# Kernel tuning notes

Measured on AMD Instinct MI355X. Metric: run time of the kernel, lower is better.

Reference implementation:

```python
import jax, jax.numpy as jnp
import numpy as np

MODEL_DIM = 2048
NUM_HEADS = 32
HEAD_DIM = 64
NUM_KV_HEADS = 8
ROPE_BASE = 10000.0
BATCH = 2
SEQ = 2048


def setup_inputs() -> dict:
    key = jax.random.key(0)
    ks = jax.random.split(key, 5)
    sd = 1.0 / np.sqrt(MODEL_DIM)
    x = jax.random.normal(ks[0], (BATCH, SEQ, MODEL_DIM), dtype=jnp.float32)
    Wq = jax.random.normal(ks[1], (MODEL_DIM, NUM_HEADS * HEAD_DIM), dtype=jnp.float32) * sd
    Wk = jax.random.normal(ks[2], (MODEL_DIM, NUM_KV_HEADS * HEAD_DIM), dtype=jnp.float32) * sd
    Wv = jax.random.normal(ks[3], (MODEL_DIM, NUM_KV_HEADS * HEAD_DIM), dtype=jnp.float32) * sd
    Wo = jax.random.normal(ks[4], (NUM_HEADS * HEAD_DIM, MODEL_DIM), dtype=jnp.float32) * sd
    return {"x": x, "Wq": Wq, "Wk": Wk, "Wv": Wv, "Wo": Wo}


def _rope_cache(seq_len, head_dim, base, dtype):
    # inv_freq over even dims, standard rotate-half (Llama-style) RoPE cache
    inv_freq = 1.0 / (base ** (jnp.arange(0, head_dim, 2, dtype=jnp.float32) / head_dim))
    t = jnp.arange(seq_len, dtype=jnp.float32)
    freqs = jnp.outer(t, inv_freq)               # [S, hd/2]
    emb = jnp.concatenate([freqs, freqs], axis=-1)  # [S, hd]
    return jnp.cos(emb).astype(dtype), jnp.sin(emb).astype(dtype)


def _rotate_half(x):
    h = x.shape[-1] // 2
    return jnp.concatenate([-x[..., h:], x[..., :h]], axis=-1)


def _apply_rope(q, k, cos, sin):
    # q,k: [B, H, S, hd]; cos,sin: [S, hd] -> broadcast over batch/heads
    cos = cos[None, None, :, :]
    sin = sin[None, None, :, :]
    q = q * cos + _rotate_half(q) * sin
    k = k * cos + _rotate_half(k) * sin
    return q, k


def reference(x, Wq, Wk, Wv, Wo):
    bsz, seq_len, _ = x.shape
    q_per_kv = NUM_HEADS // NUM_KV_HEADS

    # projections -> [B, H, S, hd]
    q = (x @ Wq).reshape(bsz, seq_len, NUM_HEADS, HEAD_DIM).transpose(0, 2, 1, 3)
    k = (x @ Wk).reshape(bsz, seq_len, NUM_KV_HEADS, HEAD_DIM).transpose(0, 2, 1, 3)
    v = (x @ Wv).reshape(bsz, seq_len, NUM_KV_HEADS, HEAD_DIM).transpose(0, 2, 1, 3)

    # GQA: repeat_interleave KV heads to match Q heads
    k = jnp.repeat(k, q_per_kv, axis=1)
    v = jnp.repeat(v, q_per_kv, axis=1)

    cos, sin = _rope_cache(seq_len, HEAD_DIM, ROPE_BASE, x.dtype)
    q, k = _apply_rope(q, k, cos, sin)

    scale = 1.0 / np.sqrt(HEAD_DIM)
    scores = jnp.einsum('bhqd,bhkd->bhqk', q, k) * scale  # [B,H,S,S]
    causal = jnp.tril(jnp.ones((seq_len, seq_len), dtype=bool))
    scores = jnp.where(causal[None, None], scores, jnp.finfo(scores.dtype).min)
    attn = jax.nn.softmax(scores, axis=-1)
    y = jnp.einsum('bhqk,bhkd->bhqd', attn, v)  # [B,H,S,hd]

    y = y.transpose(0, 2, 1, 3).reshape(bsz, seq_len, NUM_HEADS * HEAD_DIM)
    return y @ Wo
```

## Files before the change

kernel.cpp:

```cpp
#include <hip/hip_runtime.h>
#include <cstdint>

typedef unsigned short u16;
typedef __attribute__((ext_vector_type(8))) short short8;
typedef __attribute__((ext_vector_type(4))) short short4v;
typedef __attribute__((ext_vector_type(4))) float f32x4;

#define SEQ     2048
#define NHEADS  32
#define NKV     8
#define HD      64
#define DM      2048
#define MROWS   4096
#define KVSTR   1024
#define PSTR    88

__device__ __forceinline__ float b2f(unsigned int u) {
    return __builtin_bit_cast(float, u << 16);
}
__device__ __forceinline__ u16 f2b(float f) {
    unsigned int u = __builtin_bit_cast(unsigned int, f);
    return (u16)((u + 0x7fffu + ((u >> 16) & 1u)) >> 16);
}

__device__ __forceinline__ float dpp_red_max16(float x) {
    int v = __builtin_bit_cast(int, x);
    x = fmaxf(x, __builtin_bit_cast(float,
        __builtin_amdgcn_update_dpp(v, v, 0xB1, 0xF, 0xF, true)));
    v = __builtin_bit_cast(int, x);
    x = fmaxf(x, __builtin_bit_cast(float,
        __builtin_amdgcn_update_dpp(v, v, 0x4E, 0xF, 0xF, true)));
    v = __builtin_bit_cast(int, x);
    x = fmaxf(x, __builtin_bit_cast(float,
        __builtin_amdgcn_update_dpp(v, v, 0x141, 0xF, 0xF, true)));
    v = __builtin_bit_cast(int, x);
    x = fmaxf(x, __builtin_bit_cast(float,
        __builtin_amdgcn_update_dpp(v, v, 0x140, 0xF, 0xF, true)));
    return x;
}
__device__ __forceinline__ float dpp_red_sum16(float x) {
    int v = __builtin_bit_cast(int, x);
    x = x + __builtin_bit_cast(float,
        __builtin_amdgcn_update_dpp(v, v, 0xB1, 0xF, 0xF, true));
    v = __builtin_bit_cast(int, x);
    x = x + __builtin_bit_cast(float,
        __builtin_amdgcn_update_dpp(v, v, 0x4E, 0xF, 0xF, true));
    v = __builtin_bit_cast(int, x);
    x = x + __builtin_bit_cast(float,
        __builtin_amdgcn_update_dpp(v, v, 0x141, 0xF, 0xF, true));
    v = __builtin_bit_cast(int, x);
    x = x + __builtin_bit_cast(float,
        __builtin_amdgcn_update_dpp(v, v, 0x140, 0xF, 0xF, true));
    return x;
}

#define GLOAD_LDS16(g, l)                                              \
    __builtin_amdgcn_global_load_lds(                                  \
        (const __attribute__((address_space(1))) void*)(g),            \
        (__attribute__((address_space(3))) void*)(l), 16, 0, 0)

__global__ __launch_bounds__(256) void cvt_f32_bf16(
    const float* __restrict__ in, u16* __restrict__ out, int n4) {
    int i = blockIdx.x * 256 + threadIdx.x;
    if (i < n4) {
        float4 v = ((const float4*)in)[i];
        ushort4 o;
        o.x = f2b(v.x); o.y = f2b(v.y); o.z = f2b(v.z); o.w = f2b(v.w);
        ((ushort4*)out)[i] = o;
    }
}

__global__ __launch_bounds__(256) void rope_table_kernel(
    float* __restrict__ cosT, float* __restrict__ sinT) {
    int idx = blockIdx.x * 256 + threadIdx.x;
    int s  = idx >> 5;
    int dl = idx & 31;
    float inv_freq = exp2f((float)dl * -0.41524101186092025f);
    float ang = (float)s * inv_freq;
    float sn, cs;
    sincosf(ang, &sn, &cs);
    cosT[idx] = cs;
    sinT[idx] = sn;
}

__global__ __launch_bounds__(256) void transpose_f32_bf16(
    const float* __restrict__ in, u16* __restrict__ out, int K, int N) {
    __shared__ float tile[32][33];
    int n0 = blockIdx.x * 32, k0 = blockIdx.y * 32;
    int tx = threadIdx.x, ty = threadIdx.y;
    for (int r = ty; r < 32; r += 8)
        tile[r][tx] = in[(size_t)(k0 + r) * N + n0 + tx];
    __syncthreads();
    for (int r = ty; r < 32; r += 8)
        out[(size_t)(n0 + r) * K + k0 + tx] = f2b(tile[tx][r]);
}

#define GEMM_BODY(A, BT, Kdim)                                             \
    constexpr int BK = 32;                                                 \
    __shared__ __align__(16) u16 As[128 * BK];                             \
    __shared__ __align__(16) u16 Bs[128 * BK];                             \
    const int tid  = threadIdx.x;                                          \
    const int wid  = tid >> 6;                                             \
    const int lane = tid & 63;                                             \
    const int quad = lane >> 4;                                            \
    const int l16  = lane & 15;                                            \
    const int rowBase = blockIdx.y * 128;                                  \
    const int colBase = blockIdx.x * 128;                                  \
    const int wr = (wid >> 1) * 64;                                        \
    const int wc = (wid & 1) * 64;                                         \
    const int srow = wid * 32 + (lane >> 2);                               \
    const int scol = (lane & 3) * 8;                                       \
    const u16* gA = (A)  + (size_t)(rowBase + srow) * (Kdim) + scol;       \
    const u16* gB = (BT) + (size_t)(colBase + srow) * (Kdim) + scol;       \
    u16* lA0 = &As[(wid * 32) * BK];                                       \
    u16* lA1 = &As[(wid * 32 + 16) * BK];                                  \
    u16* lB0 = &Bs[(wid * 32) * BK];                                       \
    u16* lB1 = &Bs[(wid * 32 + 16) * BK];                                  \
    const size_t row16 = (size_t)16 * (Kdim);                              \
    f32x4 acc[4][4] = {};                                                  \
    for (int k0 = 0; k0 < (Kdim); k0 += BK) {                              \
        GLOAD_LDS16(gA + k0,         lA0);                                 \
        GLOAD_LDS16(gA + k0 + row16, lA1);                                 \
        GLOAD_LDS16(gB + k0,         lB0);                                 \
        GLOAD_LDS16(gB + k0 + row16, lB1);                                 \
        __syncthreads();                                                   \
        short8 a[4], b[4];                                                 \
        _Pragma("unroll")                                                  \
        for (int mi = 0; mi < 4; ++mi)                                     \
            a[mi] = *(const short8*)&As[(wr + mi * 16 + l16) * BK + quad * 8]; \
        _Pragma("unroll")                                                  \
        for (int ni = 0; ni < 4; ++ni)                                     \
            b[ni] = *(const short8*)&Bs[(wc + ni * 16 + l16) * BK + quad * 8]; \
        _Pragma("unroll")                                                  \
        for (int mi = 0; mi < 4; ++mi)                                     \
            _Pragma("unroll")                                              \
            for (int ni = 0; ni < 4; ++ni)                                 \
                acc[mi][ni] = __builtin_amdgcn_mfma_f32_16x16x32_bf16(     \
                    a[mi], b[ni], acc[mi][ni], 0, 0, 0);                   \
        __syncthreads();                                                   \
    }                                                                      \
    const int wRow = rowBase + wr;                                         \
    const int wCol = colBase + wc;

__global__ __launch_bounds__(256) void gemm_qkv(
    const u16* __restrict__ A, const u16* __restrict__ BT,
    u16* __restrict__ Qb, u16* __restrict__ KVb,
    const float* __restrict__ cosT, const float* __restrict__ sinT) {
    GEMM_BODY(A, BT, DM)

    u16* dst;
    int dstride, dcol;
    float scale;
    bool doRope;
    if (wCol < 2048)      { dst = Qb;  dstride = 2048; dcol = wCol;        scale = 0.125f; doRope = true;  }
    else if (wCol < 2560) { dst = KVb; dstride = 1024; dcol = wCol - 2048; scale = 1.0f;   doRope = true;  }
    else                  { dst = KVb; dstride = 1024; dcol = wCol - 2048; scale = 1.0f;   doRope = false; }

#pragma unroll
    for (int mi = 0; mi < 4; ++mi) {
#pragma unroll
        for (int r = 0; r < 4; ++r) {
            const int R = wRow + mi * 16 + quad * 4 + r;
            u16* crow = dst + (size_t)R * dstride + dcol;
            if (doRope) {
                const int s = R & (SEQ - 1);
#pragma unroll
                for (int ni = 0; ni < 2; ++ni) {
                    const int dl = ni * 16 + l16;
                    float lo = acc[mi][ni][r];
                    float hi = acc[mi][ni + 2][r];
                    float cs = cosT[s * 32 + dl];
                    float sn = sinT[s * 32 + dl];
                    crow[dl]      = f2b((lo * cs - hi * sn) * scale);
                    crow[dl + 32] = f2b((hi * cs + lo * sn) * scale);
                }
            } else {
#pragma unroll
                for (int ni = 0; ni < 4; ++ni)
                    crow[ni * 16 + l16] = f2b(acc[mi][ni][r]);
            }
        }
    }
}

__global__ __launch_bounds__(256) void gemm_out(
    const u16* __restrict__ A, const u16* __restrict__ BT,
    float* __restrict__ C32) {
    GEMM_BODY(A, BT, DM)
#pragma unroll
    for (int mi = 0; mi < 4; ++mi) {
#pragma unroll
        for (int r = 0; r < 4; ++r) {
            const int R = wRow + mi * 16 + quad * 4 + r;
            float* crow = C32 + (size_t)R * DM + wCol;
#pragma unroll
            for (int ni = 0; ni < 4; ++ni)
                crow[ni * 16 + l16] = acc[mi][ni][r];
        }
    }
}

__global__ __launch_bounds__(512, 4) void flash_attn(
    const u16* __restrict__ Q, const u16* __restrict__ KV,
    u16* __restrict__ Yb, float* __restrict__ PoA,
    float* __restrict__ Ml) {
    __shared__ __align__(16) u16 Ks[64 * 64];
    __shared__ __align__(16) u16 Vt[64 * 72];
    __shared__ __align__(16) u16 Ps[8 * 16 * PSTR];

    const int p   = blockIdx.x >> 1;
    const int sh  = blockIdx.x & 1;
    const int h   = blockIdx.y;
    const int b   = blockIdx.z;
    const int kvh = h >> 2;
    const int tid  = threadIdx.x;
    const int wid  = tid >> 6;
    const int lane = tid & 63;
    const int quad = lane >> 4;
    const int l16  = lane & 15;

    const u16* Kg = KV + (size_t)b * SEQ * KVSTR + kvh * HD;
    const u16* Vg = Kg + 512;
    u16* Psw = Ps + wid * 16 * PSTR;

    const int kKey = tid >> 3, kCc = tid & 7;
    const int vkp  = tid & 31;
    const int vd0  = (tid >> 5) * 4;

    for (int ph = 0; ph < 2; ++ph) {
        const int qt = ph ? (15 - p) : p;
        const int hc = ph ? (16 - p) : (p + 1);
        const int tS = sh * hc;
        const int rowBaseW = qt * 128 + wid * 16;

        short8 qf[2];
#pragma unroll
        for (int ks = 0; ks < 2; ++ks)
            qf[ks] = *(const short8*)&Q[
                (size_t)(b * SEQ + rowBaseW + l16) * (NHEADS * HD)
                + h * HD + ks * 32 + quad * 8];

        f32x4 o[4] = {};
        float mi[4], li[4];
#pragma unroll
        for (int r = 0; r < 4; ++r) { mi[r] = -3e38f; li[r] = 0.f; }

        const size_t jF = (size_t)tS * 64;
        short8  kreg = *(const short8*)&Kg[(jF + kKey) * KVSTR + kCc * 8];
        short4v vrA  = *(const short4v*)&Vg[(jF + 2 * vkp)     * KVSTR + vd0];
        short4v vrB  = *(const short4v*)&Vg[(jF + 2 * vkp + 1) * KVSTR + vd0];

        for (int tt = 0; tt < hc; ++tt) {
            const int j0 = (tS + tt) * 64;
            __syncthreads();

            *(short8*)&Ks[kKey * 64 + ((kCc ^ (kKey & 7)) * 8)] = kreg;
#pragma unroll
            for (int i = 0; i < 4; ++i) {
                unsigned int w = (unsigned int)(u16)vrA[i]
                               | ((unsigned int)(u16)vrB[i] << 16);
                ((unsigned int*)Vt)[(vd0 + i) * 36 + vkp] = w;
            }
            __syncthreads();

            if (tt + 1 < hc) {
                const size_t jn = (size_t)(j0 + 64);
                kreg = *(const short8*)&Kg[(jn + kKey) * KVSTR + kCc * 8];
                vrA  = *(const short4v*)&Vg[(jn + 2 * vkp)     * KVSTR + vd0];
                vrB  = *(const short4v*)&Vg[(jn + 2 * vkp + 1) * KVSTR + vd0];
            }

            f32x4 s[4] = {};
#pragma unroll
            for (int ks = 0; ks < 2; ++ks)
#pragma unroll
                for (int ct = 0; ct < 4; ++ct) {
                    int key = ct * 16 + l16;
                    int cc  = (ks * 4 + quad) ^ (key & 7);
                    short8 bk = *(const short8*)&Ks[key * 64 + cc * 8];
                    s[ct] = __builtin_amdgcn_mfma_f32_16x16x32_bf16(
                        qf[ks], bk, s[ct], 0, 0, 0);
                }

            if (j0 + 63 > rowBaseW) {
#pragma unroll
                for (int ct = 0; ct < 4; ++ct)
#pragma unroll
                    for (int r = 0; r < 4; ++r) {
                        int R = rowBaseW + quad * 4 + r;
                        int J = j0 + ct * 16 + l16;
                        if (J > R) s[ct][r] = -3e38f;
                    }
            }

#pragma unroll
            for (int r = 0; r < 4; ++r) {
                float rmax = fmaxf(fmaxf(s[0][r], s[1][r]),
                                   fmaxf(s[2][r], s[3][r]));
                rmax = dpp_red_max16(rmax);
                float mnew  = fmaxf(mi[r], rmax);
                float alpha = __expf(mi[r] - mnew);
                mi[r] = mnew;
                float rs = 0.f;
#pragma unroll
                for (int ct = 0; ct < 4; ++ct) {
                    float pv = __expf(s[ct][r] - mnew);
                    s[ct][r] = pv;
                    rs += pv;
                    o[ct][r] *= alpha;
                }
                rs = dpp_red_sum16(rs);
                li[r] = li[r] * alpha + rs;
            }

#pragma unroll
            for (int ct = 0; ct < 4; ++ct)
#pragma unroll
                for (int r = 0; r < 4; ++r)
                    Psw[(quad * 4 + r) * PSTR + ct * 16 + l16] = f2b(s[ct][r]);

            short8 pa[2];
#pragma unroll
            for (int ks = 0; ks < 2; ++ks)
                pa[ks] = *(const short8*)&Psw[l16 * PSTR + ks * 32 + quad * 8];
#pragma unroll
            for (int ks = 0; ks < 2; ++ks)
#pragma unroll
                for (int ct = 0; ct < 4; ++ct) {
                    short8 vbf = *(const short8*)&Vt[(ct * 16 + l16) * 72 + ks * 32 + quad * 8];
                    o[ct] = __builtin_amdgcn_mfma_f32_16x16x32_bf16(
                        pa[ks], vbf, o[ct], 0, 0, 0);
                }
        }

        float rli[4];
#pragma unroll
        for (int r = 0; r < 4; ++r)
            rli[r] = li[r] > 0.f ? 1.0f / li[r] : 0.f;
        if (sh == 0) {
#pragma unroll
            for (int r = 0; r < 4; ++r) {
                int R = rowBaseW + quad * 4 + r;
                float* arow = PoA + (size_t)(b * SEQ + R) * (NHEADS * HD) + h * HD;
#pragma unroll
                for (int ct = 0; ct < 4; ++ct)
                    arow[ct * 16 + l16] = o[ct][r] * rli[r];
            }
        } else {
#pragma unroll
            for (int r = 0; r < 4; ++r) {
                int R = rowBaseW + quad * 4 + r;
                u16* yrow = Yb + (size_t)(b * SEQ + R) * (NHEADS * HD) + h * HD;
#pragma unroll
                for (int ct = 0; ct < 4; ++ct)
                    yrow[ct * 16 + l16] = f2b(o[ct][r] * rli[r]);
            }
        }
        if (l16 == 0) {
            float2* MlX = (float2*)Ml + (size_t)sh * 131072
                        + ((b * 32 + h) * 2048 + rowBaseW + quad * 4);
#pragma unroll
            for (int r = 0; r < 4; ++r)
                MlX[r] = make_float2(mi[r], li[r]);
        }
    }
}

__global__ __launch_bounds__(256) void combine_kernel(
    const float* __restrict__ PoA, const float* __restrict__ Ml,
    u16* __restrict__ Yb) {
    const size_t e = ((size_t)blockIdx.x * 256 + threadIdx.x) * 8;
    const int rowg = (int)(e >> 11);
    const int c    = (int)(e & 2047);
    const int h    = c >> 6;
    const int bz   = rowg >> 11;
    const int row  = rowg & 2047;
    const int slot = ((bz * 32 + h) * 2048 + row) * 2;
    const float mA = Ml[slot],          lA = Ml[slot + 1];
    const float mB = Ml[262144 + slot], lB = Ml[262144 + slot + 1];
    const float m  = fmaxf(mA, mB);
    const float wA = lA * __expf(mA - m);
    const float wB = lB * __expf(mB - m);
    const float inv = 1.0f / (wA + wB);
    const float a = wA * inv, bw = wB * inv;
    float4 A0 = *(const float4*)(PoA + e);
    float4 A1 = *(const float4*)(PoA + e + 4);
    short8 Bv = *(const short8*)(Yb + e);
    float av[8] = {A0.x, A0.y, A0.z, A0.w, A1.x, A1.y, A1.z, A1.w};
    u16 yo[8];
#pragma unroll
    for (int j = 0; j < 8; ++j)
        yo[j] = f2b(a * av[j] + bw * b2f((unsigned int)(u16)Bv[j]));
    *(short8*)(Yb + e) = *(short8*)yo;
}

extern "C" void kernel_launch(void* const* d_in, const int* in_sizes, int n_in,
                              void* d_out, int out_size, void* d_ws, size_t ws_size,
                              hipStream_t stream) {
    const float* x  = (const float*)d_in[0];
    const float* Wq = (const float*)d_in[1];
    const float* Wk = (const float*)d_in[2];
    const float* Wv = (const float*)d_in[3];
    const float* Wo = (const float*)d_in[4];
    float* out = (float*)d_out;

    char* ws = (char*)d_ws;
    u16*  xb    = (u16*)(ws);
    u16*  WqkvT = (u16*)(ws + 16777216);
    u16*  WoT   = (u16*)(ws + 29360128);
    u16*  Qb    = (u16*)(ws + 37748736);
    u16*  KVb   = (u16*)(ws + 54525952);
    u16*  Yb    = (u16*)(ws + 62914560);
    float* cosT = (float*)(ws + 79691776);
    float* sinT = (float*)(ws + 79953920);
    float* PoA  = (float*)(ws);
    float* Ml   = (float*)(ws + 33554432);

    rope_table_kernel<<<dim3(65536 / 256), 256, 0, stream>>>(cosT, sinT);

    cvt_f32_bf16<<<dim3(MROWS * DM / 4 / 256), 256, 0, stream>>>(x, xb, MROWS * DM / 4);

    dim3 tb(32, 8);
    transpose_f32_bf16<<<dim3(2048/32, 2048/32), tb, 0, stream>>>(Wq, WqkvT, 2048, 2048);
    transpose_f32_bf16<<<dim3( 512/32, 2048/32), tb, 0, stream>>>(Wk, WqkvT + 2048 * 2048, 2048, 512);
    transpose_f32_bf16<<<dim3( 512/32, 2048/32), tb, 0, stream>>>(Wv, WqkvT + 2560 * 2048, 2048, 512);

    gemm_qkv<<<dim3(24, 32), 256, 0, stream>>>(xb, WqkvT, Qb, KVb, cosT, sinT);

    flash_attn<<<dim3(16, NHEADS, 2), 512, 0, stream>>>(Qb, KVb, Yb, PoA, Ml);

    combine_kernel<<<dim3(4096), 256, 0, stream>>>(PoA, Ml, Yb);

    transpose_f32_bf16<<<dim3(2048/32, 2048/32), tb, 0, stream>>>(Wo, WoT, 2048, 2048);

    gemm_out<<<dim3(16, 32), 256, 0, stream>>>(Yb, WoT, out);
}
```

Measured before the change: 376.4 us.

## Pipeline GEMM loads with 4-stage LDS ring, XOR swizzle, and MFMA priority

Replaces the single-buffered GEMM main loop with a 4-buffer LDS ring that prefetches three K-tiles ahead. Each iteration waits only on the oldest outstanding loads via a manual vmcnt and barrier, which removes one of the two barriers per iteration and overlaps global-to-LDS traffic with MFMA work. An XOR swizzle on LDS rows avoids bank conflicts, and s_setprio raises wave priority around the MFMA block. LDS use grows to 64KB per block, and launch bounds now request two blocks per CU. The hand-written waitcnt values must match the exact number of loads issued per stage.

```diff
diff --git a/kernel.cpp b/kernel.cpp
--- a/kernel.cpp
+++ b/kernel.cpp
@@ -95,54 +95,89 @@
         out[(size_t)(n0 + r) * K + k0 + tx] = f2b(tile[tx][r]);
 }
 
-#define GEMM_BODY(A, BT, Kdim)                                             \
-    constexpr int BK = 32;                                                 \
-    __shared__ __align__(16) u16 As[128 * BK];                             \
-    __shared__ __align__(16) u16 Bs[128 * BK];                             \
-    const int tid  = threadIdx.x;                                          \
-    const int wid  = tid >> 6;                                             \
-    const int lane = tid & 63;                                             \
-    const int quad = lane >> 4;                                            \
-    const int l16  = lane & 15;                                            \
-    const int rowBase = blockIdx.y * 128;                                  \
-    const int colBase = blockIdx.x * 128;                                  \
-    const int wr = (wid >> 1) * 64;                                        \
-    const int wc = (wid & 1) * 64;                                         \
-    const int srow = wid * 32 + (lane >> 2);                               \
-    const int scol = (lane & 3) * 8;                                       \
-    const u16* gA = (A)  + (size_t)(rowBase + srow) * (Kdim) + scol;       \
-    const u16* gB = (BT) + (size_t)(colBase + srow) * (Kdim) + scol;       \
-    u16* lA0 = &As[(wid * 32) * BK];                                       \
-    u16* lA1 = &As[(wid * 32 + 16) * BK];                                  \
-    u16* lB0 = &Bs[(wid * 32) * BK];                                       \
-    u16* lB1 = &Bs[(wid * 32 + 16) * BK];                                  \
-    const size_t row16 = (size_t)16 * (Kdim);                              \
-    f32x4 acc[4][4] = {};                                                  \
-    for (int k0 = 0; k0 < (Kdim); k0 += BK) {                              \
-        GLOAD_LDS16(gA + k0,         lA0);                                 \
-        GLOAD_LDS16(gA + k0 + row16, lA1);                                 \
-        GLOAD_LDS16(gB + k0,         lB0);                                 \
-        GLOAD_LDS16(gB + k0 + row16, lB1);                                 \
-        __syncthreads();                                                   \
-        short8 a[4], b[4];                                                 \
-        _Pragma("unroll")                                                  \
-        for (int mi = 0; mi < 4; ++mi)                                     \
-            a[mi] = *(const short8*)&As[(wr + mi * 16 + l16) * BK + quad * 8]; \
-        _Pragma("unroll")                                                  \
-        for (int ni = 0; ni < 4; ++ni)                                     \
-            b[ni] = *(const short8*)&Bs[(wc + ni * 16 + l16) * BK + quad * 8]; \
-        _Pragma("unroll")                                                  \
-        for (int mi = 0; mi < 4; ++mi)                                     \
-            _Pragma("unroll")                                              \
-            for (int ni = 0; ni < 4; ++ni)                                 \
-                acc[mi][ni] = __builtin_amdgcn_mfma_f32_16x16x32_bf16(     \
-                    a[mi], b[ni], acc[mi][ni], 0, 0, 0);                   \
-        __syncthreads();                                                   \
-    }                                                                      \
-    const int wRow = rowBase + wr;                                         \
+#define GEMM_BODY(Aptr, BTptr, Kdim)                                        \
+    __shared__ __align__(16) u16 rA[4][4096];                               \
+    __shared__ __align__(16) u16 rB[4][4096];                               \
+    const int tid  = threadIdx.x;                                           \
+    const int wid  = tid >> 6;                                              \
+    const int lane = tid & 63;                                              \
+    const int quad = lane >> 4;                                             \
+    const int l16  = lane & 15;                                             \
+    const int rowBase = blockIdx.y * 128;                                   \
+    const int colBase = blockIdx.x * 128;                                   \
+    const int wr = (wid >> 1) * 64;                                         \
+    const int wc = (wid & 1) * 64;                                          \
+    size_t sAoff[2], sBoff[2];                                              \
+    int ldOff[2];                                                           \
+    _Pragma("unroll")                                                       \
+    for (int j = 0; j < 2; ++j) {                                           \
+        const int p = j * 256 + tid;       \
+        const int q = p >> 3;                                               \
+        const int u = (p & 7) ^ (q & 7);               \
+        const int r = (q << 1) | (u >> 2);                                  \
+        const int sc = (u & 3) * 8;              \
+        sAoff[j] = (size_t)(rowBase + r) * (Kdim) + sc;                     \
+        sBoff[j] = (size_t)(colBase + r) * (Kdim) + sc;                     \
+        ldOff[j] = (j * 256 + (wid << 6)) * 8;    \
+    }                                                                       \
+    int aOff[4], bOff[4];                  \
+    _Pragma("unroll")                                                       \
+    for (int mi = 0; mi < 4; ++mi) {                                        \
+        const int ra = wr + mi * 16 + l16;                                  \
+        const int qa = ra >> 1;                                             \
+        const int ua = ((ra & 1) << 2) | quad;                              \
+        aOff[mi] = (qa * 8 + (ua ^ (qa & 7))) * 8;                          \
+        const int rb = wc + mi * 16 + l16;                                  \
+        const int qb = rb >> 1;                                             \
+        const int ub = ((rb & 1) << 2) | quad;                              \
+        bOff[mi] = (qb * 8 + (ub ^ (qb & 7))) * 8;                          \
+    }                                                                       \
+    f32x4 acc[4][4] = {};                                                   \
+    const int NT = (Kdim) / 32;                                             \
+    _Pragma("unroll")                                                       \
+    for (int st = 0; st < 3; ++st) {       \
+        _Pragma("unroll")                                                   \
+        for (int j = 0; j < 2; ++j) {                                       \
+            GLOAD_LDS16(Aptr  + sAoff[j] + st * 32, &rA[st][ldOff[j]]);     \
+            GLOAD_LDS16(BTptr + sBoff[j] + st * 32, &rB[st][ldOff[j]]);     \
+        }                                                                   \
+    }                                                                       \
+    for (int s = 0; s < NT; ++s) {                                          \
+        if (s < NT - 2)                                                     \
+            asm volatile("s_waitcnt vmcnt(8)\n\ts_barrier" ::: "memory");   \
+        else if (s == NT - 2)                                               \
+            asm volatile("s_waitcnt vmcnt(4)\n\ts_barrier" ::: "memory");   \
+        else                                                                \
+            asm volatile("s_waitcnt vmcnt(0)\n\ts_barrier" ::: "memory");   \
+        const u16* Ab = rA[s & 3];                                          \
+        const u16* Bb = rB[s & 3];                                          \
+        short8 a[4], b[4];                                                  \
+        _Pragma("unroll")                                                   \
+        for (int mi = 0; mi < 4; ++mi) a[mi] = *(const short8*)&Ab[aOff[mi]]; \
+        _Pragma("unroll")                                                   \
+        for (int ni = 0; ni < 4; ++ni) b[ni] = *(const short8*)&Bb[bOff[ni]]; \
+        if (s + 3 < NT) {                           \
+            const int bi = (s + 3) & 3;                                     \
+            const int kk = (s + 3) * 32;                                    \
+            _Pragma("unroll")                                               \
+            for (int j = 0; j < 2; ++j) {                                   \
+                GLOAD_LDS16(Aptr  + sAoff[j] + kk, &rA[bi][ldOff[j]]);      \
+                GLOAD_LDS16(BTptr + sBoff[j] + kk, &rB[bi][ldOff[j]]);      \
+            }                                                               \
+        }                                                                   \
+        __builtin_amdgcn_s_setprio(1);                                      \
+        _Pragma("unroll")                                                   \
+        for (int mi = 0; mi < 4; ++mi)                                      \
+            _Pragma("unroll")                                               \
+            for (int ni = 0; ni < 4; ++ni)                                  \
+                acc[mi][ni] = __builtin_amdgcn_mfma_f32_16x16x32_bf16(      \
+                    a[mi], b[ni], acc[mi][ni], 0, 0, 0);                    \
+        __builtin_amdgcn_s_setprio(0);                                      \
+    }                                                                       \
+    const int wRow = rowBase + wr;                                          \
     const int wCol = colBase + wc;
 
-__global__ __launch_bounds__(256) void gemm_qkv(
+__global__ __launch_bounds__(256, 2) void gemm_qkv(
     const u16* __restrict__ A, const u16* __restrict__ BT,
     u16* __restrict__ Qb, u16* __restrict__ KVb,
     const float* __restrict__ cosT, const float* __restrict__ sinT) {
@@ -183,7 +218,7 @@
     }
 }
 
-__global__ __launch_bounds__(256) void gemm_out(
+__global__ __launch_bounds__(256, 2) void gemm_out(
     const u16* __restrict__ A, const u16* __restrict__ BT,
     float* __restrict__ C32) {
     GEMM_BODY(A, BT, DM)
```

Result: faster. 351.7 us (-6.5%).
